# Performance work log

Measured on AMD Instinct MI355X. Metric: run time of the kernel, lower is better.

The kernel has to match this reference:

```python
import jax, jax.numpy as jnp
import numpy as np

FP, DP, K, S, B, T, H, ZD = 96, 28, 3, 4, 64, 8, 512, 2
CP = FP - DP + 1          # 69, valid cross-correlation output size
NP = CP * CP              # 4761 = num_pixels


def setup_inputs() -> dict:
    key = jax.random.key(0)
    ks = jax.random.split(key, 12)
    def rn(k, shape, s=0.02):
        return jax.random.normal(k, shape, jnp.float32) * s
    return {
        "frames": jax.random.uniform(ks[0], (S, B, T, FP, FP), jnp.float32),
        "conv_kernel": jax.random.uniform(ks[1], (S, B, K, DP, DP), jnp.float32),
        "eps": jax.random.normal(ks[2], (S, B, K, ZD), jnp.float32),
        "W1": rn(ks[3], (NP, H)), "b1": jnp.zeros((H,), jnp.float32),
        "Wm1": rn(ks[4], (H, H // 2)), "bm1": jnp.zeros((H // 2,), jnp.float32),
        "Wm2": rn(ks[5], (H // 2, ZD)), "bm2": jnp.zeros((ZD,), jnp.float32),
        "Ws1": rn(ks[6], (H, H // 2)), "bs1": jnp.zeros((H // 2,), jnp.float32),
        "Ws2": rn(ks[7], (H // 2, ZD)), "bs2": jnp.zeros((ZD,), jnp.float32),
        "timestep": 0,
    }


def _axis_weights(p, n):
    """Bilinear 1-D gather indices/weights with zero padding outside [0, n)."""
    p0 = jnp.floor(p)
    f = p - p0
    i0 = p0.astype(jnp.int32)
    i1 = i0 + 1
    w0 = jnp.where((i0 >= 0) & (i0 < n), 1.0 - f, 0.0)
    w1 = jnp.where((i1 >= 0) & (i1 < n), f, 0.0)
    return jnp.clip(i0, 0, n - 1), jnp.clip(i1, 0, n - 1), w0, w1


def _place_digit(digit, zw):
    """AT.digit_to_frame: place DPxDP digit into FPxFP frame at z_where (torch
    affine_grid/grid_sample, align_corners=False, zero padding). theta scale =
    FP/DP, translation = -z_where*FP/DP, i.e. in_coord = (FP/DP)*(out - zw)."""
    scale = FP / DP
    out_c = (2.0 * jnp.arange(FP, dtype=jnp.float32) + 1.0) / FP - 1.0  # (FP,)
    px = ((scale * (out_c - zw[0]) + 1.0) * DP - 1.0) * 0.5  # x source pix
    py = ((scale * (out_c - zw[1]) + 1.0) * DP - 1.0) * 0.5  # y source pix
    y0, y1, wy0, wy1 = _axis_weights(py, DP)
    x0, x1, wx0, wx1 = _axis_weights(px, DP)
    # separable bilinear: interp rows then cols
    tmp = wy0[:, None] * digit[y0, :] + wy1[:, None] * digit[y1, :]  # (FP,DP)
    return wx0[None, :] * tmp[:, x0] + wx1[None, :] * tmp[:, x1]     # (FP,FP)

_place_batch = jax.vmap(_place_digit)


def reference(frames, conv_kernel, eps, W1, b1, Wm1, bm1, Wm2, bm2,
              Ws1, bs1, Ws2, bs2, timestep):
    SB = S * B
    frame_left = frames[:, :, timestep]  # (S,B,FP,FP)
    means, stds, zs = [], [], []
    for k in range(K):
        # per-sample dynamic-kernel cross-correlation via grouped conv
        lhs = frame_left.reshape(1, SB, FP, FP)
        rhs = conv_kernel[:, :, k].reshape(SB, 1, DP, DP)
        conved = jax.lax.conv_general_dilated(
            lhs, rhs, (1, 1), 'VALID', feature_group_count=SB)  # (1,SB,CP,CP)
        scores = jax.nn.softmax(conved.reshape(S, B, NP), axis=-1)
        h = jax.nn.relu(scores @ W1 + b1)                       # (S,B,H)
        mean_k = jnp.tanh(jax.nn.relu(h @ Wm1 + bm1) @ Wm2 + bm2)
        std_k = jnp.exp(jax.nn.relu(h @ Ws1 + bs1) @ Ws2 + bs2)
        z_k = mean_k + std_k * eps[:, :, k]                     # rsample
        recon = _place_batch(conv_kernel[:, :, k].reshape(SB, DP, DP),
                             z_k.reshape(SB, ZD)).reshape(S, B, FP, FP)
        frame_left = frame_left - recon
        means.append(mean_k); stds.append(std_k); zs.append(z_k)
    q_mean = jnp.stack(means, 2)    # (S,B,K,2)
    q_std = jnp.stack(stds, 2)
    z_where = jnp.stack(zs, 2)
    return jnp.stack([q_mean, q_std, z_where], 0)  # (3,S,B,K,2)
```

## Files before the change

### kernel.cpp

```cpp
#include <hip/hip_runtime.h>
#include <hip/hip_bf16.h>
#include <math.h>

#define FPD 96
#define DPD 28
#define CPD 69
#define NPD 4761
#define KKC 3
#define SBN 256
#define TT 8
#define HD 512
#define ZDD 2
#define KPAD 4768
#define SPLITK 15
#define FRSH 104
#define CVS 76

typedef __attribute__((ext_vector_type(8))) short bf16x8;
typedef __attribute__((ext_vector_type(4))) float f32x4;
typedef _Float16 half_t;
typedef __attribute__((ext_vector_type(2))) _Float16 half2_t;

__device__ __forceinline__ float bf2f_lo(unsigned int u) {
    union { unsigned int i; float f; } v; v.i = u << 16; return v.f;
}
__device__ __forceinline__ float bf2f_hi(unsigned int u) {
    union { unsigned int i; float f; } v; v.i = u & 0xffff0000u; return v.f;
}
__device__ __forceinline__ half2_t u2h(unsigned int u) {
    union { unsigned int i; half2_t h; } v; v.i = u; return v.h;
}

__global__ __launch_bounds__(256) void wprep_kernel(
    const float* __restrict__ W1, const float* __restrict__ Wm1,
    const float* __restrict__ Ws1,
    ushort* __restrict__ W1T, ushort* __restrict__ WhidT)
{
    __shared__ ushort tile[64][65];
    const int t = threadIdx.x;
    const int ln = t & 63;
    const int lr = t >> 6;
    const int b = blockIdx.x;

    if (b < 600) {
        const int k0 = (b % 75) * 64;
        const int n0 = (b / 75) * 64;
        #pragma unroll
        for (int i = 0; i < 16; ++i) {
            int kk = k0 + lr + i * 4;
            float v = (kk < NPD) ? W1[(size_t)kk * HD + n0 + ln] : 0.f;
            __hip_bfloat16 h = __float2bfloat16(v);
            tile[lr + i * 4][ln] = *reinterpret_cast<ushort*>(&h);
        }
        __syncthreads();
        #pragma unroll
        for (int i = 0; i < 16; ++i) {
            int nn = lr + i * 4;
            int kk = k0 + ln;
            if (kk < KPAD)
                W1T[(size_t)(n0 + nn) * KPAD + kk] = tile[ln][nn];
        }
    } else {
        const int bb = b - 600;
        const int i0 = (bb & 7) * 64;
        const int r0 = (bb >> 3) * 64;
        #pragma unroll
        for (int rep = 0; rep < 16; ++rep) {
            int i = i0 + lr + rep * 4;
            int r = r0 + ln;
            const float* src = (r >= 256) ? Ws1 : Wm1;
            float v = src[(size_t)i * 256 + (r & 255)];
            __hip_bfloat16 h = __float2bfloat16(v);
            tile[lr + rep * 4][ln] = *reinterpret_cast<ushort*>(&h);
        }
        __syncthreads();
        #pragma unroll
        for (int rep = 0; rep < 16; ++rep) {
            int r = r0 + lr + rep * 4;
            WhidT[(size_t)r * 512 + i0 + ln] = tile[ln][lr + rep * 4];
        }
    }
}

__global__ __launch_bounds__(1024, 4) void conv_softmax_kernel(
    const float* __restrict__ frames, const int* __restrict__ tsp,
    float* __restrict__ frameL, const float* __restrict__ ck,
    const float* __restrict__ z_cur,
    ushort* __restrict__ e_buf, float* __restrict__ inv_denom, int k)
{
    __shared__ __align__(16) half_t fr[96 * FRSH];
    __shared__ __align__(16) half_t kr[28 * 32];
    __shared__ float dg[784];
    __shared__ __align__(16) float cv[4][69 * CVS];
    __shared__ float red[32];

    const int t = threadIdx.x;
    const int ib = blockIdx.x;

    if (t < 28 * 32) {
        int dy = t >> 5, dx = t & 31;
        float v = (dx < 28) ? ck[((size_t)ib * KKC + k) * 784 + dy * 28 + dx] : 0.f;
        kr[t] = (half_t)v;
    }
    if (k > 0 && t < 784) dg[t] = ck[((size_t)ib * KKC + (k - 1)) * 784 + t];
    float zx = 0.f, zy = 0.f;
    if (k > 0) { zx = z_cur[ib * 2]; zy = z_cur[ib * 2 + 1]; }
    __syncthreads();

    const float* src = (k < 2)
        ? frames + ((size_t)ib * TT + *tsp) * 9216
        : frameL + (size_t)ib * 9216;
    const float scale = 96.f / 28.f;
    for (int p = t; p < 9216; p += 1024) {
        int r = p / 96, c = p - r * 96;
        float val = src[p];
        if (k > 0) {
            float oci = (2.f * r + 1.f) / 96.f - 1.f;
            float ocj = (2.f * c + 1.f) / 96.f - 1.f;
            float py = ((scale * (oci - zy) + 1.f) * 28.f - 1.f) * 0.5f;
            float px = ((scale * (ocj - zx) + 1.f) * 28.f - 1.f) * 0.5f;
            float py0f = floorf(py), px0f = floorf(px);
            float fy = py - py0f, fx = px - px0f;
            int y0 = (int)py0f, x0 = (int)px0f;
            int y1 = y0 + 1, x1 = x0 + 1;
            float wy0 = (y0 >= 0 && y0 < DPD) ? 1.f - fy : 0.f;
            float wy1 = (y1 >= 0 && y1 < DPD) ? fy : 0.f;
            float wx0 = (x0 >= 0 && x0 < DPD) ? 1.f - fx : 0.f;
            float wx1 = (x1 >= 0 && x1 < DPD) ? fx : 0.f;
            int y0c = min(max(y0, 0), DPD - 1), y1c = min(max(y1, 0), DPD - 1);
            int x0c = min(max(x0, 0), DPD - 1), x1c = min(max(x1, 0), DPD - 1);
            float tmp0 = wy0 * dg[y0c * DPD + x0c] + wy1 * dg[y1c * DPD + x0c];
            float tmp1 = wy0 * dg[y0c * DPD + x1c] + wy1 * dg[y1c * DPD + x1c];
            val -= wx0 * tmp0 + wx1 * tmp1;
        }
        fr[r * FRSH + c] = (half_t)val;
        if (k == 1) frameL[(size_t)ib * 9216 + p] = val;
    }
    if (t < 96 * 8) fr[(t >> 3) * FRSH + 96 + (t & 7)] = (half_t)0.f;
    __syncthreads();

    if (t < 828) {
        const int q    = t / 207;
        const int rem  = t - q * 207;
        const int tile = rem / 69;
        const int oy   = rem - tile * 69;
        const int ox0  = tile * 24;
        const int dy0  = q * 7;

        float acc[24];
        #pragma unroll
        for (int j = 0; j < 24; ++j) acc[j] = 0.f;

        #pragma unroll 1
        for (int dd = 0; dd < 7; ++dd) {
            const int dy = dy0 + dd;
            const unsigned int* frow = (const unsigned int*)&fr[(oy + dy) * FRSH + ox0];
            const unsigned int* krow = (const unsigned int*)&kr[dy * 32];
            unsigned int W[28], K[16], V[25];
            #pragma unroll
            for (int u = 0; u < 7; ++u) {
                uint4 v = *(const uint4*)(frow + 4 * u);
                W[4*u] = v.x; W[4*u+1] = v.y; W[4*u+2] = v.z; W[4*u+3] = v.w;
            }
            #pragma unroll
            for (int u = 0; u < 4; ++u) {
                uint4 v = *(const uint4*)(krow + 4 * u);
                K[4*u] = v.x; K[4*u+1] = v.y; K[4*u+2] = v.z; K[4*u+3] = v.w;
            }
            #pragma unroll
            for (int i = 0; i < 25; ++i)
                V[i] = (W[i] >> 16) | (W[i + 1] << 16);
            #pragma unroll
            for (int m = 0; m < 12; ++m) {
                float ae = acc[2*m], ao = acc[2*m+1];
                #pragma unroll
                for (int i = 0; i < 14; ++i) {
                    ae = __builtin_amdgcn_fdot2(u2h(W[m + i]), u2h(K[i]), ae, false);
                    ao = __builtin_amdgcn_fdot2(u2h(V[m + i]), u2h(K[i]), ao, false);
                }
                acc[2*m] = ae; acc[2*m+1] = ao;
            }
        }
        float* cvq = &cv[q][oy * CVS + ox0];
        #pragma unroll
        for (int u = 0; u < 6; ++u) {
            float4 v = make_float4(acc[4*u], acc[4*u+1], acc[4*u+2], acc[4*u+3]);
            *(float4*)(cvq + 4 * u) = v;
        }
    }
    __syncthreads();

    float m = -INFINITY;
    for (int p = t; p < 69 * CVS; p += 1024) {
        int ox = p - (p / CVS) * CVS;
        if (ox < CPD) {
            float v = cv[0][p] + cv[1][p] + cv[2][p] + cv[3][p];
            cv[0][p] = v;
            m = fmaxf(m, v);
        }
    }
    #pragma unroll
    for (int off = 32; off > 0; off >>= 1) m = fmaxf(m, __shfl_down(m, off, 64));
    int lane = t & 63, wid = t >> 6;
    if (lane == 0) red[wid] = m;
    __syncthreads();
    m = red[0];
    #pragma unroll
    for (int i = 1; i < 16; ++i) m = fmaxf(m, red[i]);

    float s = 0.f;
    ushort* eo = e_buf + (size_t)ib * KPAD;
    for (int p = t; p < 69 * CVS; p += 1024) {
        int oy = p / CVS;
        int ox = p - oy * CVS;
        if (ox < CPD) {
            float ev = __expf(cv[0][p] - m);
            __hip_bfloat16 h = __float2bfloat16(ev);
            eo[oy * CPD + ox] = *reinterpret_cast<ushort*>(&h);
            s += ev;
        }
    }
    #pragma unroll
    for (int off = 32; off > 0; off >>= 1) s += __shfl_down(s, off, 64);
    if (lane == 0) red[16 + wid] = s;
    __syncthreads();
    if (t == 0) {
        float tot = 0.f;
        #pragma unroll
        for (int i = 0; i < 16; ++i) tot += red[16 + i];
        inv_denom[ib] = 1.0f / tot;
    }
    if (t < KPAD - NPD) eo[NPD + t] = 0;
}

__global__ __launch_bounds__(256) void gemm1_mfma(
    const ushort* __restrict__ E, const ushort* __restrict__ W1T,
    float* __restrict__ Cpart)
{
    __shared__ __align__(16) ushort As[64][56];
    __shared__ __align__(16) ushort Bs[64][56];

    const int t  = threadIdx.x;
    const int m0 = blockIdx.x * 64;
    const int n0 = blockIdx.y * 64;
    const int z  = blockIdx.z;
    const int step0 = z * 10;
    const int nstep = min(10, 149 - step0);

    const int r = t >> 2;
    const int c = t & 3;
    const int l = t & 63;
    const int w = t >> 6;
    const int lm = l & 15;
    const int kb = l >> 4;

    f32x4 zero = {0.f, 0.f, 0.f, 0.f};
    f32x4 acc[4] = {zero, zero, zero, zero};

    const ushort* eA = E   + (size_t)(m0 + r) * KPAD + c * 8;
    const ushort* eB = W1T + (size_t)(n0 + r) * KPAD + c * 8;

    int k0 = step0 * 32;
    float4 av = *(const float4*)(eA + k0);
    float4 bv = *(const float4*)(eB + k0);

    for (int s = 0; s < nstep; ++s) {
        *(float4*)&As[r][c * 8] = av;
        *(float4*)&Bs[r][c * 8] = bv;
        __syncthreads();
        if (s + 1 < nstep) {
            int kn = (step0 + s + 1) * 32;
            av = *(const float4*)(eA + kn);
            bv = *(const float4*)(eB + kn);
        }
        bf16x8 a = *(const bf16x8*)&As[w * 16 + lm][kb * 8];
        #pragma unroll
        for (int j = 0; j < 4; ++j) {
            bf16x8 b = *(const bf16x8*)&Bs[j * 16 + lm][kb * 8];
            acc[j] = __builtin_amdgcn_mfma_f32_16x16x32_bf16(a, b, acc[j], 0, 0, 0);
        }
        __syncthreads();
    }

    const int mrow = m0 + w * 16 + kb * 4;
    #pragma unroll
    for (int j = 0; j < 4; ++j) {
        int n = n0 + j * 16 + lm;
        #pragma unroll
        for (int rg = 0; rg < 4; ++rg)
            Cpart[((size_t)z * SBN + mrow + rg) * HD + n] = acc[j][rg];
    }
}

__global__ __launch_bounds__(512) void mlp_fused(
    const float* __restrict__ Cpart, const float* __restrict__ inv_denom,
    const float* __restrict__ b1, const ushort* __restrict__ WhidT,
    const float* __restrict__ bm1, const float* __restrict__ bs1,
    const float* __restrict__ Wm2, const float* __restrict__ bm2,
    const float* __restrict__ Ws2, const float* __restrict__ bs2,
    const float* __restrict__ eps, float* __restrict__ out,
    float* __restrict__ z_cur, int k)
{
    __shared__ float hsh[HD];
    __shared__ float h2[2][256];
    __shared__ float res_sh[2][2];

    const int t = threadIdx.x;
    const int ib = blockIdx.x;

    {
        float s = 0.f;
        #pragma unroll
        for (int z = 0; z < SPLITK; ++z)
            s += Cpart[((size_t)z * SBN + ib) * HD + t];
        hsh[t] = fmaxf(fmaf(s, inv_denom[ib], b1[t]), 0.f);
    }
    __syncthreads();

    {
        int head = t >> 8, col = t & 255;
        const uint4* Wr = (const uint4*)(WhidT + (size_t)(head * 256 + col) * 512);
        float bias = head ? bs1[col] : bm1[col];
        float a = 0.f;
        #pragma unroll 8
        for (int u = 0; u < 64; ++u) {
            uint4 wv = Wr[u];
            const float* hp = &hsh[u * 8];
            a = fmaf(hp[0], bf2f_lo(wv.x), a);
            a = fmaf(hp[1], bf2f_hi(wv.x), a);
            a = fmaf(hp[2], bf2f_lo(wv.y), a);
            a = fmaf(hp[3], bf2f_hi(wv.y), a);
            a = fmaf(hp[4], bf2f_lo(wv.z), a);
            a = fmaf(hp[5], bf2f_hi(wv.z), a);
            a = fmaf(hp[6], bf2f_lo(wv.w), a);
            a = fmaf(hp[7], bf2f_hi(wv.w), a);
        }
        h2[head][col] = fmaxf(a + bias, 0.f);
    }
    __syncthreads();

    {
        int w = t >> 6, l = t & 63;
        if (w < 4) {
            int zd = (w >> 1) & 1, head = w & 1;
            const float* W2 = head ? Ws2 : Wm2;
            float a = 0.f;
            #pragma unroll
            for (int u = 0; u < 4; ++u) {
                int i = l + u * 64;
                a = fmaf(h2[head][i], W2[i * 2 + zd], a);
            }
            #pragma unroll
            for (int off = 32; off > 0; off >>= 1) a += __shfl_down(a, off, 64);
            if (l == 0) {
                float r = head ? __expf(a + bs2[zd]) : tanhf(a + bm2[zd]);
                res_sh[zd][head] = r;
            }
        }
    }
    __syncthreads();
    if (t < 2) {
        int zd = t;
        float mean = res_sh[zd][0];
        float stdv = res_sh[zd][1];
        float ev = eps[(size_t)ib * 6 + k * 2 + zd];
        float z = fmaf(stdv, ev, mean);
        int oidx = ib * 6 + k * 2 + zd;
        out[oidx]        = mean;
        out[1536 + oidx] = stdv;
        out[3072 + oidx] = z;
        z_cur[ib * 2 + zd] = z;
    }
}

extern "C" void kernel_launch(void* const* d_in, const int* in_sizes, int n_in,
                              void* d_out, int out_size, void* d_ws, size_t ws_size,
                              hipStream_t stream)
{
    const float* frames = (const float*)d_in[0];
    const float* ck     = (const float*)d_in[1];
    const float* eps    = (const float*)d_in[2];
    const float* W1     = (const float*)d_in[3];
    const float* b1     = (const float*)d_in[4];
    const float* Wm1    = (const float*)d_in[5];
    const float* bm1    = (const float*)d_in[6];
    const float* Wm2    = (const float*)d_in[7];
    const float* bm2    = (const float*)d_in[8];
    const float* Ws1    = (const float*)d_in[9];
    const float* bs1    = (const float*)d_in[10];
    const float* Ws2    = (const float*)d_in[11];
    const float* bs2    = (const float*)d_in[12];
    const int*   tsp    = (const int*)d_in[13];
    float* out = (float*)d_out;

    float* frameL  = (float*)d_ws;
    float* Cpart   = frameL + 2359296;
    float* inv_den = Cpart + 1966080;
    float* z_cur   = inv_den + 256;
    ushort* e_buf  = (ushort*)(z_cur + 512);
    ushort* W1T    = e_buf + (size_t)SBN * KPAD;
    ushort* WhidT  = W1T + (size_t)HD * KPAD;

    wprep_kernel<<<664, 256, 0, stream>>>(W1, Wm1, Ws1, W1T, WhidT);

    for (int k = 0; k < KKC; ++k) {
        conv_softmax_kernel<<<256, 1024, 0, stream>>>(
            frames, tsp, frameL, ck, z_cur, e_buf, inv_den, k);
        gemm1_mfma<<<dim3(4, 8, SPLITK), 256, 0, stream>>>(e_buf, W1T, Cpart);
        mlp_fused<<<256, 512, 0, stream>>>(Cpart, inv_den, b1, WhidT,
                                           bm1, bs1, Wm2, bm2, Ws2, bs2,
                                           eps, out, z_cur, k);
    }
}
```

Baseline: 301.3 us.

## Fuse all stages into one cooperative persistent kernel with grid syncs

Replaces the weight-prep kernel and the per-step conv/softmax, GEMM and MLP launches (ten launches) with a single cooperative kernel of 256 blocks. Stages are separated by grid.sync() and share a single shared-memory arena. The split-K GEMM is reorganized so each of the 256 blocks computes a 64x64 tile over 640 K (SPLITK 8, KPAD padded to 5120). This removes launch overhead and inter-kernel gaps, at the cost of grid-wide barriers and a GEMM mapping constrained to the block count.

```diff
diff --git a/kernel.cpp b/kernel.cpp
--- a/kernel.cpp
+++ b/kernel.cpp
@@ -1,6 +1,9 @@
 #include <hip/hip_runtime.h>
 #include <hip/hip_bf16.h>
+#include <hip/hip_cooperative_groups.h>
 #include <math.h>
+
+namespace cg = cooperative_groups;
 
 #define FPD 96
 #define DPD 28
@@ -10,9 +13,8 @@
 #define SBN 256
 #define TT 8
 #define HD 512
-#define ZDD 2
-#define KPAD 4768
-#define SPLITK 15
+#define KPAD 5120
+#define SPLITK 8
 #define FRSH 104
 #define CVS 76
 
@@ -30,346 +32,340 @@
 __device__ __forceinline__ half2_t u2h(unsigned int u) {
     union { unsigned int i; half2_t h; } v; v.i = u; return v.h;
 }
-
-__global__ __launch_bounds__(256) void wprep_kernel(
-    const float* __restrict__ W1, const float* __restrict__ Wm1,
-    const float* __restrict__ Ws1,
-    ushort* __restrict__ W1T, ushort* __restrict__ WhidT)
+__device__ __forceinline__ ushort f2bf(float f) {
+    __hip_bfloat16 h = __float2bfloat16(f);
+    return *reinterpret_cast<ushort*>(&h);
+}
+
+__global__ __launch_bounds__(1024, 4) void mega_kernel(
+    const float* __restrict__ frames, const float* __restrict__ ck,
+    const float* __restrict__ eps, const float* __restrict__ W1,
+    const float* __restrict__ b1,
+    const float* __restrict__ Wm1, const float* __restrict__ bm1,
+    const float* __restrict__ Wm2, const float* __restrict__ bm2,
+    const float* __restrict__ Ws1, const float* __restrict__ bs1,
+    const float* __restrict__ Ws2, const float* __restrict__ bs2,
+    const int* __restrict__ tsp, float* __restrict__ out,
+    float* __restrict__ frameL, float* __restrict__ Cpart,
+    float* __restrict__ inv_denom, float* __restrict__ z_cur,
+    ushort* __restrict__ e_buf, ushort* __restrict__ W1T,
+    ushort* __restrict__ WhidT)
 {
-    __shared__ ushort tile[64][65];
+    __shared__ __align__(16) char arena[108928];
+    cg::grid_group grid = cg::this_grid();
     const int t = threadIdx.x;
-    const int ln = t & 63;
-    const int lr = t >> 6;
     const int b = blockIdx.x;
-
-    if (b < 600) {
-        const int k0 = (b % 75) * 64;
-        const int n0 = (b / 75) * 64;
-        #pragma unroll
-        for (int i = 0; i < 16; ++i) {
-            int kk = k0 + lr + i * 4;
-            float v = (kk < NPD) ? W1[(size_t)kk * HD + n0 + ln] : 0.f;
-            __hip_bfloat16 h = __float2bfloat16(v);
-            tile[lr + i * 4][ln] = *reinterpret_cast<ushort*>(&h);
+    const int ib = b;
+
+    {
+        const int g = t >> 8, t2 = t & 255;
+        const int ln = t2 & 63, lr = t2 >> 6;
+        ushort (*tile)[65] = (ushort(*)[65])(arena + g * 8320);
+        const int job = b * 4 + g;
+        if (job < 640) {
+            const int k0 = (job % 80) * 64;
+            const int n0 = (job / 80) * 64;
+            #pragma unroll
+            for (int i = 0; i < 16; ++i) {
+                int kk = k0 + lr + i * 4;
+                float v = (kk < NPD) ? W1[(size_t)kk * HD + n0 + ln] : 0.f;
+                tile[lr + i * 4][ln] = f2bf(v);
+            }
+        } else if (job < 704) {
+            const int j2 = job - 640;
+            const int i0 = (j2 & 7) * 64;
+            const int r0 = (j2 >> 3) * 64;
+            #pragma unroll
+            for (int rep = 0; rep < 16; ++rep) {
+                int i = i0 + lr + rep * 4;
+                int r = r0 + ln;
+                const float* src = (r >= 256) ? Ws1 : Wm1;
+                tile[lr + rep * 4][ln] = f2bf(src[(size_t)i * 256 + (r & 255)]);
+            }
         }
         __syncthreads();
-        #pragma unroll
-        for (int i = 0; i < 16; ++i) {
-            int nn = lr + i * 4;
-            int kk = k0 + ln;
-            if (kk < KPAD)
-                W1T[(size_t)(n0 + nn) * KPAD + kk] = tile[ln][nn];
-        }
-    } else {
-        const int bb = b - 600;
-        const int i0 = (bb & 7) * 64;
-        const int r0 = (bb >> 3) * 64;
-        #pragma unroll
-        for (int rep = 0; rep < 16; ++rep) {
-            int i = i0 + lr + rep * 4;
-            int r = r0 + ln;
-            const float* src = (r >= 256) ? Ws1 : Wm1;
-            float v = src[(size_t)i * 256 + (r & 255)];
-            __hip_bfloat16 h = __float2bfloat16(v);
-            tile[lr + rep * 4][ln] = *reinterpret_cast<ushort*>(&h);
-        }
-        __syncthreads();
-        #pragma unroll
-        for (int rep = 0; rep < 16; ++rep) {
-            int r = r0 + lr + rep * 4;
-            WhidT[(size_t)r * 512 + i0 + ln] = tile[ln][lr + rep * 4];
-        }
-    }
-}
-
-__global__ __launch_bounds__(1024, 4) void conv_softmax_kernel(
-    const float* __restrict__ frames, const int* __restrict__ tsp,
-    float* __restrict__ frameL, const float* __restrict__ ck,
-    const float* __restrict__ z_cur,
-    ushort* __restrict__ e_buf, float* __restrict__ inv_denom, int k)
-{
-    __shared__ __align__(16) half_t fr[96 * FRSH];
-    __shared__ __align__(16) half_t kr[28 * 32];
-    __shared__ float dg[784];
-    __shared__ __align__(16) float cv[4][69 * CVS];
-    __shared__ float red[32];
-
-    const int t = threadIdx.x;
-    const int ib = blockIdx.x;
-
-    if (t < 28 * 32) {
-        int dy = t >> 5, dx = t & 31;
-        float v = (dx < 28) ? ck[((size_t)ib * KKC + k) * 784 + dy * 28 + dx] : 0.f;
-        kr[t] = (half_t)v;
-    }
-    if (k > 0 && t < 784) dg[t] = ck[((size_t)ib * KKC + (k - 1)) * 784 + t];
-    float zx = 0.f, zy = 0.f;
-    if (k > 0) { zx = z_cur[ib * 2]; zy = z_cur[ib * 2 + 1]; }
-    __syncthreads();
-
-    const float* src = (k < 2)
-        ? frames + ((size_t)ib * TT + *tsp) * 9216
-        : frameL + (size_t)ib * 9216;
-    const float scale = 96.f / 28.f;
-    for (int p = t; p < 9216; p += 1024) {
-        int r = p / 96, c = p - r * 96;
-        float val = src[p];
-        if (k > 0) {
-            float oci = (2.f * r + 1.f) / 96.f - 1.f;
-            float ocj = (2.f * c + 1.f) / 96.f - 1.f;
-            float py = ((scale * (oci - zy) + 1.f) * 28.f - 1.f) * 0.5f;
-            float px = ((scale * (ocj - zx) + 1.f) * 28.f - 1.f) * 0.5f;
-            float py0f = floorf(py), px0f = floorf(px);
-            float fy = py - py0f, fx = px - px0f;
-            int y0 = (int)py0f, x0 = (int)px0f;
-            int y1 = y0 + 1, x1 = x0 + 1;
-            float wy0 = (y0 >= 0 && y0 < DPD) ? 1.f - fy : 0.f;
-            float wy1 = (y1 >= 0 && y1 < DPD) ? fy : 0.f;
-            float wx0 = (x0 >= 0 && x0 < DPD) ? 1.f - fx : 0.f;
-            float wx1 = (x1 >= 0 && x1 < DPD) ? fx : 0.f;
-            int y0c = min(max(y0, 0), DPD - 1), y1c = min(max(y1, 0), DPD - 1);
-            int x0c = min(max(x0, 0), DPD - 1), x1c = min(max(x1, 0), DPD - 1);
-            float tmp0 = wy0 * dg[y0c * DPD + x0c] + wy1 * dg[y1c * DPD + x0c];
-            float tmp1 = wy0 * dg[y0c * DPD + x1c] + wy1 * dg[y1c * DPD + x1c];
-            val -= wx0 * tmp0 + wx1 * tmp1;
-        }
-        fr[r * FRSH + c] = (half_t)val;
-        if (k == 1) frameL[(size_t)ib * 9216 + p] = val;
-    }
-    if (t < 96 * 8) fr[(t >> 3) * FRSH + 96 + (t & 7)] = (half_t)0.f;
-    __syncthreads();
-
-    if (t < 828) {
-        const int q    = t / 207;
-        const int rem  = t - q * 207;
-        const int tile = rem / 69;
-        const int oy   = rem - tile * 69;
-        const int ox0  = tile * 24;
-        const int dy0  = q * 7;
-
-        float acc[24];
-        #pragma unroll
-        for (int j = 0; j < 24; ++j) acc[j] = 0.f;
-
-        #pragma unroll 1
-        for (int dd = 0; dd < 7; ++dd) {
-            const int dy = dy0 + dd;
-            const unsigned int* frow = (const unsigned int*)&fr[(oy + dy) * FRSH + ox0];
-            const unsigned int* krow = (const unsigned int*)&kr[dy * 32];
-            unsigned int W[28], K[16], V[25];
-            #pragma unroll
-            for (int u = 0; u < 7; ++u) {
-                uint4 v = *(const uint4*)(frow + 4 * u);
-                W[4*u] = v.x; W[4*u+1] = v.y; W[4*u+2] = v.z; W[4*u+3] = v.w;
-            }
-            #pragma unroll
-            for (int u = 0; u < 4; ++u) {
-                uint4 v = *(const uint4*)(krow + 4 * u);
-                K[4*u] = v.x; K[4*u+1] = v.y; K[4*u+2] = v.z; K[4*u+3] = v.w;
-            }
-            #pragma unroll
-            for (int i = 0; i < 25; ++i)
-                V[i] = (W[i] >> 16) | (W[i + 1] << 16);
-            #pragma unroll
-            for (int m = 0; m < 12; ++m) {
-                float ae = acc[2*m], ao = acc[2*m+1];
-                #pragma unroll
-                for (int i = 0; i < 14; ++i) {
-                    ae = __builtin_amdgcn_fdot2(u2h(W[m + i]), u2h(K[i]), ae, false);
-                    ao = __builtin_amdgcn_fdot2(u2h(V[m + i]), u2h(K[i]), ao, false);
-                }
-                acc[2*m] = ae; acc[2*m+1] = ao;
-            }
-        }
-        float* cvq = &cv[q][oy * CVS + ox0];
-        #pragma unroll
-        for (int u = 0; u < 6; ++u) {
-            float4 v = make_float4(acc[4*u], acc[4*u+1], acc[4*u+2], acc[4*u+3]);
-            *(float4*)(cvq + 4 * u) = v;
-        }
-    }
-    __syncthreads();
-
-    float m = -INFINITY;
-    for (int p = t; p < 69 * CVS; p += 1024) {
-        int ox = p - (p / CVS) * CVS;
-        if (ox < CPD) {
-            float v = cv[0][p] + cv[1][p] + cv[2][p] + cv[3][p];
-            cv[0][p] = v;
-            m = fmaxf(m, v);
-        }
-    }
-    #pragma unroll
-    for (int off = 32; off > 0; off >>= 1) m = fmaxf(m, __shfl_down(m, off, 64));
-    int lane = t & 63, wid = t >> 6;
-    if (lane == 0) red[wid] = m;
-    __syncthreads();
-    m = red[0];
-    #pragma unroll
-    for (int i = 1; i < 16; ++i) m = fmaxf(m, red[i]);
-
-    float s = 0.f;
-    ushort* eo = e_buf + (size_t)ib * KPAD;
-    for (int p = t; p < 69 * CVS; p += 1024) {
-        int oy = p / CVS;
-        int ox = p - oy * CVS;
-        if (ox < CPD) {
-            float ev = __expf(cv[0][p] - m);
-            __hip_bfloat16 h = __float2bfloat16(ev);
-            eo[oy * CPD + ox] = *reinterpret_cast<ushort*>(&h);
-            s += ev;
-        }
-    }
-    #pragma unroll
-    for (int off = 32; off > 0; off >>= 1) s += __shfl_down(s, off, 64);
-    if (lane == 0) red[16 + wid] = s;
-    __syncthreads();
-    if (t == 0) {
-        float tot = 0.f;
-        #pragma unroll
-        for (int i = 0; i < 16; ++i) tot += red[16 + i];
-        inv_denom[ib] = 1.0f / tot;
-    }
-    if (t < KPAD - NPD) eo[NPD + t] = 0;
-}
-
-__global__ __launch_bounds__(256) void gemm1_mfma(
-    const ushort* __restrict__ E, const ushort* __restrict__ W1T,
-    float* __restrict__ Cpart)
-{
-    __shared__ __align__(16) ushort As[64][56];
-    __shared__ __align__(16) ushort Bs[64][56];
-
-    const int t  = threadIdx.x;
-    const int m0 = blockIdx.x * 64;
-    const int n0 = blockIdx.y * 64;
-    const int z  = blockIdx.z;
-    const int step0 = z * 10;
-    const int nstep = min(10, 149 - step0);
-
-    const int r = t >> 2;
-    const int c = t & 3;
-    const int l = t & 63;
-    const int w = t >> 6;
-    const int lm = l & 15;
-    const int kb = l >> 4;
-
-    f32x4 zero = {0.f, 0.f, 0.f, 0.f};
-    f32x4 acc[4] = {zero, zero, zero, zero};
-
-    const ushort* eA = E   + (size_t)(m0 + r) * KPAD + c * 8;
-    const ushort* eB = W1T + (size_t)(n0 + r) * KPAD + c * 8;
-
-    int k0 = step0 * 32;
-    float4 av = *(const float4*)(eA + k0);
-    float4 bv = *(const float4*)(eB + k0);
-
-    for (int s = 0; s < nstep; ++s) {
-        *(float4*)&As[r][c * 8] = av;
-        *(float4*)&Bs[r][c * 8] = bv;
-        __syncthreads();
-        if (s + 1 < nstep) {
-            int kn = (step0 + s + 1) * 32;
-            av = *(const float4*)(eA + kn);
-            bv = *(const float4*)(eB + kn);
-        }
-        bf16x8 a = *(const bf16x8*)&As[w * 16 + lm][kb * 8];
-        #pragma unroll
-        for (int j = 0; j < 4; ++j) {
-            bf16x8 b = *(const bf16x8*)&Bs[j * 16 + lm][kb * 8];
-            acc[j] = __builtin_amdgcn_mfma_f32_16x16x32_bf16(a, b, acc[j], 0, 0, 0);
+        if (job < 640) {
+            const int k0 = (job % 80) * 64;
+            const int n0 = (job / 80) * 64;
+            #pragma unroll
+            for (int i = 0; i < 16; ++i) {
+                int nn = lr + i * 4;
+                W1T[(size_t)(n0 + nn) * KPAD + k0 + ln] = tile[ln][nn];
+            }
+        } else if (job < 704) {
+            const int j2 = job - 640;
+            const int i0 = (j2 & 7) * 64;
+            const int r0 = (j2 >> 3) * 64;
+            #pragma unroll
+            for (int rep = 0; rep < 16; ++rep) {
+                int r = r0 + lr + rep * 4;
+                WhidT[(size_t)r * 512 + i0 + ln] = tile[ln][lr + rep * 4];
+            }
         }
         __syncthreads();
     }
 
-    const int mrow = m0 + w * 16 + kb * 4;
-    #pragma unroll
-    for (int j = 0; j < 4; ++j) {
-        int n = n0 + j * 16 + lm;
-        #pragma unroll
-        for (int rg = 0; rg < 4; ++rg)
-            Cpart[((size_t)z * SBN + mrow + rg) * HD + n] = acc[j][rg];
-    }
-}
-
-__global__ __launch_bounds__(512) void mlp_fused(
-    const float* __restrict__ Cpart, const float* __restrict__ inv_denom,
-    const float* __restrict__ b1, const ushort* __restrict__ WhidT,
-    const float* __restrict__ bm1, const float* __restrict__ bs1,
-    const float* __restrict__ Wm2, const float* __restrict__ bm2,
-    const float* __restrict__ Ws2, const float* __restrict__ bs2,
-    const float* __restrict__ eps, float* __restrict__ out,
-    float* __restrict__ z_cur, int k)
-{
-    __shared__ float hsh[HD];
-    __shared__ float h2[2][256];
-    __shared__ float res_sh[2][2];
-
-    const int t = threadIdx.x;
-    const int ib = blockIdx.x;
-
-    {
-        float s = 0.f;
-        #pragma unroll
-        for (int z = 0; z < SPLITK; ++z)
-            s += Cpart[((size_t)z * SBN + ib) * HD + t];
-        hsh[t] = fmaxf(fmaf(s, inv_denom[ib], b1[t]), 0.f);
-    }
-    __syncthreads();
-
-    {
-        int head = t >> 8, col = t & 255;
-        const uint4* Wr = (const uint4*)(WhidT + (size_t)(head * 256 + col) * 512);
-        float bias = head ? bs1[col] : bm1[col];
-        float a = 0.f;
-        #pragma unroll 8
-        for (int u = 0; u < 64; ++u) {
-            uint4 wv = Wr[u];
-            const float* hp = &hsh[u * 8];
-            a = fmaf(hp[0], bf2f_lo(wv.x), a);
-            a = fmaf(hp[1], bf2f_hi(wv.x), a);
-            a = fmaf(hp[2], bf2f_lo(wv.y), a);
-            a = fmaf(hp[3], bf2f_hi(wv.y), a);
-            a = fmaf(hp[4], bf2f_lo(wv.z), a);
-            a = fmaf(hp[5], bf2f_hi(wv.z), a);
-            a = fmaf(hp[6], bf2f_lo(wv.w), a);
-            a = fmaf(hp[7], bf2f_hi(wv.w), a);
+    for (int k = 0; k < KKC; ++k) {
+        {
+            half_t* fr  = (half_t*)arena;
+            half_t* kr  = (half_t*)(arena + 19968);
+            float*  dgp = (float*)(arena + 21760);
+            float*  cvb = (float*)(arena + 24896);
+            float*  red = (float*)(arena + 108800);
+
+            if (t < 28 * 32) {
+                int dy = t >> 5, dx = t & 31;
+                float v = (dx < 28) ? ck[((size_t)ib * KKC + k) * 784 + dy * 28 + dx] : 0.f;
+                kr[t] = (half_t)v;
+            }
+            if (k > 0 && t < 784) dgp[t] = ck[((size_t)ib * KKC + (k - 1)) * 784 + t];
+            float zx = 0.f, zy = 0.f;
+            if (k > 0) { zx = z_cur[ib * 2]; zy = z_cur[ib * 2 + 1]; }
+            __syncthreads();
+
+            const float* src = (k < 2)
+                ? frames + ((size_t)ib * TT + *tsp) * 9216
+                : frameL + (size_t)ib * 9216;
+            const float scale = 96.f / 28.f;
+            for (int p = t; p < 9216; p += 1024) {
+                int r = p / 96, c = p - r * 96;
+                float val = src[p];
+                if (k > 0) {
+                    float oci = (2.f * r + 1.f) / 96.f - 1.f;
+                    float ocj = (2.f * c + 1.f) / 96.f - 1.f;
+                    float py = ((scale * (oci - zy) + 1.f) * 28.f - 1.f) * 0.5f;
+                    float px = ((scale * (ocj - zx) + 1.f) * 28.f - 1.f) * 0.5f;
+                    float py0f = floorf(py), px0f = floorf(px);
+                    float fy = py - py0f, fx = px - px0f;
+                    int y0 = (int)py0f, x0 = (int)px0f;
+                    int y1 = y0 + 1, x1 = x0 + 1;
+                    float wy0 = (y0 >= 0 && y0 < DPD) ? 1.f - fy : 0.f;
+                    float wy1 = (y1 >= 0 && y1 < DPD) ? fy : 0.f;
+                    float wx0 = (x0 >= 0 && x0 < DPD) ? 1.f - fx : 0.f;
+                    float wx1 = (x1 >= 0 && x1 < DPD) ? fx : 0.f;
+                    int y0c = min(max(y0, 0), DPD - 1), y1c = min(max(y1, 0), DPD - 1);
+                    int x0c = min(max(x0, 0), DPD - 1), x1c = min(max(x1, 0), DPD - 1);
+                    float tmp0 = wy0 * dgp[y0c * DPD + x0c] + wy1 * dgp[y1c * DPD + x0c];
+                    float tmp1 = wy0 * dgp[y0c * DPD + x1c] + wy1 * dgp[y1c * DPD + x1c];
+                    val -= wx0 * tmp0 + wx1 * tmp1;
+                }
+                fr[r * FRSH + c] = (half_t)val;
+                if (k == 1) frameL[(size_t)ib * 9216 + p] = val;
+            }
+            if (t < 96 * 8) fr[(t >> 3) * FRSH + 96 + (t & 7)] = (half_t)0.f;
+            __syncthreads();
+
+            if (t < 828) {
+                const int q    = t / 207;
+                const int rem  = t - q * 207;
+                const int tile = rem / 69;
+                const int oy   = rem - tile * 69;
+                const int ox0  = tile * 24;
+                const int dy0  = q * 7;
+
+                float acc[24];
+                #pragma unroll
+                for (int j = 0; j < 24; ++j) acc[j] = 0.f;
+
+                #pragma unroll 1
+                for (int dd = 0; dd < 7; ++dd) {
+                    const int dy = dy0 + dd;
+                    const unsigned int* frow = (const unsigned int*)&fr[(oy + dy) * FRSH + ox0];
+                    const unsigned int* krow = (const unsigned int*)&kr[dy * 32];
+                    unsigned int W[28], K[16], V[25];
+                    #pragma unroll
+                    for (int u = 0; u < 7; ++u) {
+                        uint4 v = *(const uint4*)(frow + 4 * u);
+                        W[4*u] = v.x; W[4*u+1] = v.y; W[4*u+2] = v.z; W[4*u+3] = v.w;
+                    }
+                    #pragma unroll
+                    for (int u = 0; u < 4; ++u) {
+                        uint4 v = *(const uint4*)(krow + 4 * u);
+                        K[4*u] = v.x; K[4*u+1] = v.y; K[4*u+2] = v.z; K[4*u+3] = v.w;
+                    }
+                    #pragma unroll
+                    for (int i = 0; i < 25; ++i)
+                        V[i] = (W[i] >> 16) | (W[i + 1] << 16);
+                    #pragma unroll
+                    for (int m = 0; m < 12; ++m) {
+                        float ae = acc[2*m], ao = acc[2*m+1];
+                        #pragma unroll
+                        for (int i = 0; i < 14; ++i) {
+                            ae = __builtin_amdgcn_fdot2(u2h(W[m + i]), u2h(K[i]), ae, false);
+                            ao = __builtin_amdgcn_fdot2(u2h(V[m + i]), u2h(K[i]), ao, false);
+                        }
+                        acc[2*m] = ae; acc[2*m+1] = ao;
+                    }
+                }
+                float* cvq = cvb + q * 5244 + oy * CVS + ox0;
+                #pragma unroll
+                for (int u = 0; u < 6; ++u) {
+                    float4 v = make_float4(acc[4*u], acc[4*u+1], acc[4*u+2], acc[4*u+3]);
+                    *(float4*)(cvq + 4 * u) = v;
+                }
+            }
+            __syncthreads();
+
+            float m = -INFINITY;
+            for (int p = t; p < 69 * CVS; p += 1024) {
+                int ox = p - (p / CVS) * CVS;
+                if (ox < CPD) {
+                    float v = cvb[p] + cvb[5244 + p] + cvb[2*5244 + p] + cvb[3*5244 + p];
+                    cvb[p] = v;
+                    m = fmaxf(m, v);
+                }
+            }
+            #pragma unroll
+            for (int off = 32; off > 0; off >>= 1) m = fmaxf(m, __shfl_down(m, off, 64));
+            int lane = t & 63, wid = t >> 6;
+            if (lane == 0) red[wid] = m;
+            __syncthreads();
+            m = red[0];
+            #pragma unroll
+            for (int i = 1; i < 16; ++i) m = fmaxf(m, red[i]);
+
+            float s = 0.f;
+            ushort* eo = e_buf + (size_t)ib * KPAD;
+            for (int p = t; p < 69 * CVS; p += 1024) {
+                int oy = p / CVS;
+                int ox = p - oy * CVS;
+                if (ox < CPD) {
+                    float ev = __expf(cvb[p] - m);
+                    eo[oy * CPD + ox] = f2bf(ev);
+                    s += ev;
+                }
+            }
+            #pragma unroll
+            for (int off = 32; off > 0; off >>= 1) s += __shfl_down(s, off, 64);
+            if (lane == 0) red[16 + wid] = s;
+            __syncthreads();
+            if (t == 0) {
+                float tot = 0.f;
+                #pragma unroll
+                for (int i = 0; i < 16; ++i) tot += red[16 + i];
+                inv_denom[ib] = 1.0f / tot;
+            }
+            if (t < KPAD - NPD) eo[NPD + t] = 0;
         }
-        h2[head][col] = fmaxf(a + bias, 0.f);
-    }
-    __syncthreads();
-
-    {
-        int w = t >> 6, l = t & 63;
-        if (w < 4) {
-            int zd = (w >> 1) & 1, head = w & 1;
-            const float* W2 = head ? Ws2 : Wm2;
-            float a = 0.f;
-            #pragma unroll
-            for (int u = 0; u < 4; ++u) {
-                int i = l + u * 64;
-                a = fmaf(h2[head][i], W2[i * 2 + zd], a);
-            }
-            #pragma unroll
-            for (int off = 32; off > 0; off >>= 1) a += __shfl_down(a, off, 64);
-            if (l == 0) {
-                float r = head ? __expf(a + bs2[zd]) : tanhf(a + bm2[zd]);
-                res_sh[zd][head] = r;
-            }
+
+        grid.sync();
+
+        {
+            ushort* As = (ushort*)arena;
+            ushort* Bs = As + 4608;
+
+            const int m0 = (b & 3) * 64;
+            const int n0 = ((b >> 2) & 7) * 64;
+            const int z  = b >> 5;
+            const int kbase = z * 640;
+
+            const int l  = t & 63, w = t >> 6;
+            const int wm = w & 3, wn = w >> 2;
+            const int lm = l & 15, kb = l >> 4;
+
+            const int sr = (t & 511) >> 3;
+            const int sc = (t & 7) * 8;
+            const ushort* gsrc = (t < 512)
+                ? e_buf + (size_t)(m0 + sr) * KPAD + sc
+                : W1T   + (size_t)(n0 + sr) * KPAD + sc;
+            ushort* ldst = As + (t < 512 ? 0 : 4608) + sr * 72 + sc;
+
+            f32x4 acc = {0.f, 0.f, 0.f, 0.f};
+            float4 av = *(const float4*)(gsrc + kbase);
+
+            #pragma unroll 1
+            for (int s = 0; s < 10; ++s) {
+                *(float4*)ldst = av;
+                __syncthreads();
+                if (s < 9) av = *(const float4*)(gsrc + kbase + (s + 1) * 64);
+                #pragma unroll
+                for (int ks = 0; ks < 2; ++ks) {
+                    bf16x8 a = *(const bf16x8*)(As + (wm * 16 + lm) * 72 + ks * 32 + kb * 8);
+                    bf16x8 bb = *(const bf16x8*)(Bs + (wn * 16 + lm) * 72 + ks * 32 + kb * 8);
+                    acc = __builtin_amdgcn_mfma_f32_16x16x32_bf16(a, bb, acc, 0, 0, 0);
+                }
+                __syncthreads();
+            }
+
+            const int mrow = m0 + wm * 16 + kb * 4;
+            const int ncol = n0 + wn * 16 + lm;
+            #pragma unroll
+            for (int rg = 0; rg < 4; ++rg)
+                Cpart[((size_t)z * SBN + mrow + rg) * HD + ncol] = acc[rg];
         }
-    }
-    __syncthreads();
-    if (t < 2) {
-        int zd = t;
-        float mean = res_sh[zd][0];
-        float stdv = res_sh[zd][1];
-        float ev = eps[(size_t)ib * 6 + k * 2 + zd];
-        float z = fmaf(stdv, ev, mean);
-        int oidx = ib * 6 + k * 2 + zd;
-        out[oidx]        = mean;
-        out[1536 + oidx] = stdv;
-        out[3072 + oidx] = z;
-        z_cur[ib * 2 + zd] = z;
+
+        grid.sync();
+
+        {
+            float* hsh = (float*)arena;
+            float* h2b = (float*)(arena + 2048);
+            float* res = (float*)(arena + 4096);
+
+            if (t < 512) {
+                float s = 0.f;
+                #pragma unroll
+                for (int z = 0; z < SPLITK; ++z)
+                    s += Cpart[((size_t)z * SBN + ib) * HD + t];
+                hsh[t] = fmaxf(fmaf(s, inv_denom[ib], b1[t]), 0.f);
+            }
+            __syncthreads();
+
+            if (t < 512) {
+                int head = t >> 8, col = t & 255;
+                const uint4* Wr = (const uint4*)(WhidT + (size_t)(head * 256 + col) * 512);
+                float bias = head ? bs1[col] : bm1[col];
+                float a = 0.f;
+                #pragma unroll 8
+                for (int u = 0; u < 64; ++u) {
+                    uint4 wv = Wr[u];
+                    const float* hp = &hsh[u * 8];
+                    a = fmaf(hp[0], bf2f_lo(wv.x), a);
+                    a = fmaf(hp[1], bf2f_hi(wv.x), a);
+                    a = fmaf(hp[2], bf2f_lo(wv.y), a);
+                    a = fmaf(hp[3], bf2f_hi(wv.y), a);
+                    a = fmaf(hp[4], bf2f_lo(wv.z), a);
+                    a = fmaf(hp[5], bf2f_hi(wv.z), a);
+                    a = fmaf(hp[6], bf2f_lo(wv.w), a);
+                    a = fmaf(hp[7], bf2f_hi(wv.w), a);
+                }
+                h2b[head * 256 + col] = fmaxf(a + bias, 0.f);
+            }
+            __syncthreads();
+
+            {
+                int w = t >> 6, l = t & 63;
+                if (w < 4) {
+                    int zd = (w >> 1) & 1, head = w & 1;
+                    const float* W2 = head ? Ws2 : Wm2;
+                    float a = 0.f;
+                    #pragma unroll
+                    for (int u = 0; u < 4; ++u) {
+                        int i = l + u * 64;
+                        a = fmaf(h2b[head * 256 + i], W2[i * 2 + zd], a);
+                    }
+                    #pragma unroll
+                    for (int off = 32; off > 0; off >>= 1) a += __shfl_down(a, off, 64);
+                    if (l == 0) {
+                        float r = head ? __expf(a + bs2[zd]) : tanhf(a + bm2[zd]);
+                        res[zd * 2 + head] = r;
+                    }
+                }
+            }
+            __syncthreads();
+            if (t < 2) {
+                int zd = t;
+                float mean = res[zd * 2 + 0];
+                float stdv = res[zd * 2 + 1];
+                float ev = eps[(size_t)ib * 6 + k * 2 + zd];
+                float z = fmaf(stdv, ev, mean);
+                int oidx = ib * 6 + k * 2 + zd;
+                out[oidx]        = mean;
+                out[1536 + oidx] = stdv;
+                out[3072 + oidx] = z;
+                z_cur[ib * 2 + zd] = z;
+            }
+            __syncthreads();
+        }
     }
 }
 
@@ -395,20 +391,20 @@
 
     float* frameL  = (float*)d_ws;
     float* Cpart   = frameL + 2359296;
-    float* inv_den = Cpart + 1966080;
+    float* inv_den = Cpart + 1048576;
     float* z_cur   = inv_den + 256;
     ushort* e_buf  = (ushort*)(z_cur + 512);
     ushort* W1T    = e_buf + (size_t)SBN * KPAD;
     ushort* WhidT  = W1T + (size_t)HD * KPAD;
 
-    wprep_kernel<<<664, 256, 0, stream>>>(W1, Wm1, Ws1, W1T, WhidT);
-
-    for (int k = 0; k < KKC; ++k) {
-        conv_softmax_kernel<<<256, 1024, 0, stream>>>(
-            frames, tsp, frameL, ck, z_cur, e_buf, inv_den, k);
-        gemm1_mfma<<<dim3(4, 8, SPLITK), 256, 0, stream>>>(e_buf, W1T, Cpart);
-        mlp_fused<<<256, 512, 0, stream>>>(Cpart, inv_den, b1, WhidT,
-                                           bm1, bs1, Wm2, bm2, Ws2, bs2,
-                                           eps, out, z_cur, k);
-    }
-}
+    void* args[] = {
+        (void*)&frames, (void*)&ck, (void*)&eps, (void*)&W1, (void*)&b1,
+        (void*)&Wm1, (void*)&bm1, (void*)&Wm2, (void*)&bm2,
+        (void*)&Ws1, (void*)&bs1, (void*)&Ws2, (void*)&bs2,
+        (void*)&tsp, (void*)&out,
+        (void*)&frameL, (void*)&Cpart, (void*)&inv_den, (void*)&z_cur,
+        (void*)&e_buf, (void*)&W1T, (void*)&WhidT
+    };
+    hipLaunchCooperativeKernel((const void*)mega_kernel,
+                               dim3(SBN), dim3(1024), args, 0, stream);
+}
```

New measurement: 521.9 us. +73.2%, slower.
